# Performance work log

Hardware: AMD Instinct MI355X
Metric: run time of the kernel (lower is better)

The kernel has to match this reference:

```python
import jax, jax.numpy as jnp
import numpy as np

NUM_VIEW = 300
NUM_ANGLE = 12
NUM_DEPTH = 4
GRASP_MAX_WIDTH = 0.1
B, C, NS, NG = 2, 512, 2048, 2000


def generate_grasp_views(N=NUM_VIEW):
    phi = (np.sqrt(5.0) - 1.0) / 2.0  # fibonacci sphere
    idxs = jnp.arange(N, dtype=jnp.float32)
    Z = (2.0 * idxs + 1.0) / N - 1.0
    r = jnp.sqrt(jnp.maximum(1.0 - Z * Z, 0.0))
    X = r * jnp.cos(2.0 * jnp.pi * idxs * phi)
    Y = r * jnp.sin(2.0 * jnp.pi * idxs * phi)
    return jnp.stack([X, Y, Z], -1)  # [N,3]


def viewpoint_params_to_matrix(towards, angle):
    # towards [...,3], angle [...]
    ax = towards
    zero = jnp.zeros_like(ax[..., 0])
    ay = jnp.stack([-ax[..., 1], ax[..., 0], zero], -1)
    ynorm = jnp.linalg.norm(ay, axis=-1, keepdims=True)
    ay = jnp.where(ynorm == 0, jnp.array([0.0, 1.0, 0.0], ax.dtype), ay)
    ax = ax / jnp.linalg.norm(ax, axis=-1, keepdims=True)
    ay = ay / jnp.linalg.norm(ay, axis=-1, keepdims=True)
    az = jnp.cross(ax, ay)
    c, s = jnp.cos(angle), jnp.sin(angle)
    one = jnp.ones_like(c)
    R1 = jnp.stack([one, zero * 0 + jnp.zeros_like(c), jnp.zeros_like(c),
                    jnp.zeros_like(c), c, -s,
                    jnp.zeros_like(c), s, c], -1).reshape(angle.shape + (3, 3))
    R2 = jnp.stack([ax, ay, az], -1)  # axes as columns
    return R2 @ R1


def conv1d(x, w, b):
    # 1x1 Conv1d == channel matmul. x [B,Ci,N], w [Co,Ci]
    return jnp.einsum('oi,bin->bon', w, x) + b[None, :, None]


def knn1(q, ref):
    # K=1 nearest neighbor indices of q [Nq,3] in ref [Nr,3]
    d = (jnp.sum(q * q, -1, keepdims=True) + jnp.sum(ref * ref, -1)[None, :]
         - 2.0 * q @ ref.T)
    return jnp.argmin(d, axis=-1)


def normalize_tensor(t, eps=1e-8):
    mx = jnp.max(t, -1, keepdims=True)
    mn = jnp.min(t, -1, keepdims=True)
    return (t - mn) / (mx - mn + eps)


def _process_one(seed_xyz, pose, gpoints, gscores, gwidths, views, views_rot):
    R, t = pose[:, :3], pose[:, 3]
    gp_trans = gpoints @ R.T + t                      # [Ng,3]
    gv_trans = views @ R.T                            # [V,3]
    gv_rot_trans = jnp.einsum('ij,vjk->vik', R, views_rot)  # [V,3,3]
    view_inds = knn1(views, gv_trans)                 # [V]
    gv_rot_trans = gv_rot_trans[view_inds]            # [V,3,3]
    nn_inds = knn1(seed_xyz, gp_trans)                # [Ns]
    gp_out = gp_trans[nn_inds]                        # [Ns,3]
    # gather seed dim first (Ns<Ng) then reindex views; axes independent
    sc = gscores[nn_inds][:, view_inds]               # [Ns,V,A,D]
    wd = gwidths[nn_inds][:, view_inds]
    rot = jnp.broadcast_to(gv_rot_trans[None], (seed_xyz.shape[0],) + gv_rot_trans.shape)
    return gp_out, rot, sc, wd


def setup_inputs() -> dict:
    key = jax.random.key(0)
    ks = jax.random.split(key, 16)
    seed_features = jax.random.normal(ks[0], (B, C, NS), jnp.float32)
    point_clouds = jax.random.normal(ks[1], (B, NS, 3), jnp.float32) * 0.2
    Rq = np.linalg.qr(np.asarray(jax.random.normal(ks[2], (B, 3, 3))))[0].astype(np.float32)
    trans = jax.random.normal(ks[3], (B, 3, 1), jnp.float32) * 0.1
    object_pose = jnp.concatenate([jnp.asarray(Rq), trans], -1)  # [B,3,4]
    grasp_points = jax.random.normal(ks[4], (B, NG, 3), jnp.float32) * 0.2
    grasp_labels = jax.random.uniform(ks[5], (B, NG, NUM_VIEW, NUM_ANGLE, NUM_DEPTH)) * 1.2 - 0.2
    grasp_offsets = jax.random.uniform(ks[6], (B, NG, NUM_VIEW, NUM_ANGLE, NUM_DEPTH)) * 0.15
    w = lambda k, co, ci: jax.random.normal(k, (co, ci), jnp.float32) * 0.05
    bz = lambda co: jnp.zeros((co,), jnp.float32)
    return {
        'seed_features': seed_features, 'point_clouds': point_clouds,
        'object_pose': object_pose, 'grasp_points': grasp_points,
        'grasp_labels': grasp_labels, 'grasp_offsets': grasp_offsets,
        'aw1_w': w(ks[7], C, C), 'aw1_b': bz(C),
        'aw2_w': w(ks[8], C, C), 'aw2_b': bz(C),
        'aw3_w': w(ks[9], NUM_VIEW, C), 'aw3_b': bz(NUM_VIEW),
        'sw1_w': w(ks[10], C, C), 'sw1_b': bz(C),
        'sw2_w': w(ks[11], NUM_DEPTH * NUM_ANGLE * 2, C), 'sw2_b': bz(NUM_DEPTH * NUM_ANGLE * 2),
    }


def reference(seed_features, point_clouds, object_pose, grasp_points,
              grasp_labels, grasp_offsets, aw1_w, aw1_b, aw2_w, aw2_b,
              aw3_w, aw3_b, sw1_w, sw1_b, sw2_w, sw2_b):
    Bx, Cx, Ns = seed_features.shape
    # --- ApproachNet (eval branch) ---
    res = jax.nn.relu(conv1d(seed_features, aw1_w, aw1_b))
    res = jax.nn.relu(conv1d(res, aw2_w, aw2_b))
    view_scores = conv1d(res, aw3_w, aw3_b).transpose(0, 2, 1)  # [B,Ns,V]
    top_view_inds = jnp.argmax(view_scores, -1)                 # [B,Ns]
    views = generate_grasp_views(NUM_VIEW)
    vp_xyz = views[top_view_inds]                               # [B,Ns,3]
    vp_rot = viewpoint_params_to_matrix(-vp_xyz, jnp.zeros(vp_xyz.shape[:-1], vp_xyz.dtype))
    # --- SWADNet ---
    f = jax.nn.relu(conv1d(res, sw1_w, sw1_b))
    f = conv1d(f, sw2_w, sw2_b)
    f = f.reshape(Bx, 2, NUM_ANGLE, NUM_DEPTH, Ns).transpose(0, 1, 4, 2, 3)
    grasp_score_pred = f[:, 0]   # [B,Ns,A,D]
    grasp_width_pred = f[:, 1]
    # --- process_grasp_labels (vmapped over batch) ---
    views_rot = viewpoint_params_to_matrix(-views, jnp.zeros((NUM_VIEW,), views.dtype))
    gp, rot, sc, wd = jax.vmap(_process_one, in_axes=(0, 0, 0, 0, 0, None, None))(
        point_clouds, object_pose, grasp_points, grasp_labels, grasp_offsets, views, views_rot)
    gmask = (sc <= 0.6) & (sc > 0)
    graspness = normalize_tensor(
        gmask.astype(jnp.float32).reshape(Bx, Ns, NUM_VIEW, -1).mean(-1))  # [B,Ns,V]
    label_mask = (sc > 0) & (wd <= GRASP_MAX_WIDTH)
    sc = jnp.where(label_mask, sc, 0.0)
    # --- match_grasp_view_and_label ---
    bi = jnp.arange(Bx)[:, None]
    ni = jnp.arange(Ns)[None, :]
    top_rot = rot[bi, ni, top_view_inds]  # [B,Ns,3,3]
    top_sc = sc[bi, ni, top_view_inds]    # [B,Ns,A,D]
    top_wd = wd[bi, ni, top_view_inds]
    u_max = jnp.max(top_sc)
    po = top_sc > 0
    safe = jnp.where(po, top_sc, 1.0)
    u_min = jnp.min(jnp.where(po, top_sc, jnp.inf))
    new_sc = jnp.log(u_max / safe) / (jnp.log(u_max / u_min) + 1e-8)
    top_sc = jnp.where(po, new_sc, top_sc)
    return (view_scores, vp_rot, grasp_score_pred, grasp_width_pred,
            top_rot, top_sc, top_wd, graspness, gp)
```

## Files before the change

kernel.cpp:

```cpp
#include <hip/hip_runtime.h>
#include <math.h>

#define NV 300
#define NA 12
#define ND 4
#define NB 2
#define NC 512
#define NSD 2048
#define NGP 2000
#define ROWLEN 14400

__global__ void k_setup(float* __restrict__ views, float* __restrict__ views_rot,
                        int* __restrict__ mmx) {
  int i = threadIdx.x;
  if (i == 0) { mmx[0] = 0; mmx[1] = 0x7f800000; }
  if (i >= NV) return;
  float fi = (float)i;
  float Z = (2.0f * fi + 1.0f) / 300.0f - 1.0f;
  float r = sqrtf(fmaxf(1.0f - Z * Z, 0.0f));
  float ang = (6.28318530717958647692f * fi) * 0.61803398874989484820f;
  float X = r * cosf(ang);
  float Y = r * sinf(ang);
  views[i * 3 + 0] = X; views[i * 3 + 1] = Y; views[i * 3 + 2] = Z;
  float ax0 = -X, ax1 = -Y, ax2 = -Z;
  float ay0 = -ax1, ay1 = ax0, ay2 = 0.f;
  float ynorm = sqrtf(ay0 * ay0 + ay1 * ay1 + ay2 * ay2);
  if (ynorm == 0.f) { ay0 = 0.f; ay1 = 1.f; ay2 = 0.f; }
  float an = sqrtf(ax0 * ax0 + ax1 * ax1 + ax2 * ax2);
  ax0 /= an; ax1 /= an; ax2 /= an;
  float ayn = sqrtf(ay0 * ay0 + ay1 * ay1 + ay2 * ay2);
  ay0 /= ayn; ay1 /= ayn; ay2 /= ayn;
  float az0 = ax1 * ay2 - ax2 * ay1;
  float az1 = ax2 * ay0 - ax0 * ay2;
  float az2 = ax0 * ay1 - ax1 * ay0;
  float* m = views_rot + i * 9;
  m[0] = ax0; m[1] = ay0; m[2] = az0;
  m[3] = ax1; m[4] = ay1; m[5] = az1;
  m[6] = ax2; m[7] = ay2; m[8] = az2;
}

__global__ void __launch_bounds__(512) k_batch_setup(
    const float* __restrict__ pose, const float* __restrict__ views,
    const float* __restrict__ views_rot, int* __restrict__ view_inds,
    float* __restrict__ Rsel) {
  int b = blockIdx.x, tid = threadIdx.x;
  __shared__ float R[9];
  __shared__ float gv[NV][3];
  __shared__ float gvr[NV];
  if (tid < 9) R[tid] = pose[b * 12 + (tid / 3) * 4 + (tid % 3)];
  __syncthreads();
  if (tid < NV) {
    float vx = views[tid * 3], vy = views[tid * 3 + 1], vz = views[tid * 3 + 2];
    float x = R[0] * vx + R[1] * vy + R[2] * vz;
    float y = R[3] * vx + R[4] * vy + R[5] * vz;
    float z = R[6] * vx + R[7] * vy + R[8] * vz;
    gv[tid][0] = x; gv[tid][1] = y; gv[tid][2] = z;
    gvr[tid] = x * x + y * y + z * z;
  }
  __syncthreads();
  if (tid < NV) {
    float qx = views[tid * 3], qy = views[tid * 3 + 1], qz = views[tid * 3 + 2];
    float qq = qx * qx + qy * qy + qz * qz;
    float best = INFINITY; int bi = 0;
    for (int u = 0; u < NV; u++) {
      float dot = qx * gv[u][0] + qy * gv[u][1] + qz * gv[u][2];
      float d = qq + gvr[u] - 2.f * dot;
      if (d < best) { best = d; bi = u; }
    }
    view_inds[b * NV + tid] = bi;
    const float* vr = views_rot + bi * 9;
    float* o = Rsel + (b * NV + tid) * 9;
    for (int i = 0; i < 3; i++)
      for (int j = 0; j < 3; j++)
        o[i * 3 + j] = R[i * 3 + 0] * vr[0 + j] + R[i * 3 + 1] * vr[3 + j] + R[i * 3 + 2] * vr[6 + j];
  }
}

__global__ void k_gp_trans(const float* __restrict__ pose,
                           const float* __restrict__ gpoints,
                           float* __restrict__ gpt, float* __restrict__ grr) {
  int idx = blockIdx.x * 256 + threadIdx.x;
  if (idx >= NB * NGP) return;
  int b = idx / NGP;
  const float* P = pose + b * 12;
  float px = gpoints[(size_t)idx * 3 + 0];
  float py = gpoints[(size_t)idx * 3 + 1];
  float pz = gpoints[(size_t)idx * 3 + 2];
  float x = P[0] * px + P[1] * py + P[2] * pz + P[3];
  float y = P[4] * px + P[5] * py + P[6] * pz + P[7];
  float z = P[8] * px + P[9] * py + P[10] * pz + P[11];
  gpt[(size_t)idx * 3 + 0] = x;
  gpt[(size_t)idx * 3 + 1] = y;
  gpt[(size_t)idx * 3 + 2] = z;
  grr[idx] = x * x + y * y + z * z;
}

__global__ void __launch_bounds__(256) k_nn(
    const float* __restrict__ pc, const float* __restrict__ gpt,
    const float* __restrict__ grr, int* __restrict__ nn_inds,
    float* __restrict__ out_gp) {
  int b = blockIdx.y;
  int s = blockIdx.x * 256 + threadIdx.x;
  __shared__ float gx[NGP], gy[NGP], gz[NGP], gr[NGP];
  for (int i = threadIdx.x; i < NGP; i += 256) {
    gx[i] = gpt[((size_t)b * NGP + i) * 3 + 0];
    gy[i] = gpt[((size_t)b * NGP + i) * 3 + 1];
    gz[i] = gpt[((size_t)b * NGP + i) * 3 + 2];
    gr[i] = grr[b * NGP + i];
  }
  __syncthreads();
  float qx = pc[((size_t)b * NSD + s) * 3 + 0];
  float qy = pc[((size_t)b * NSD + s) * 3 + 1];
  float qz = pc[((size_t)b * NSD + s) * 3 + 2];
  float qq = qx * qx + qy * qy + qz * qz;
  float best = INFINITY; int bi = 0;
  for (int i = 0; i < NGP; i++) {
    float dot = qx * gx[i] + qy * gy[i] + qz * gz[i];
    float d = qq + gr[i] - 2.f * dot;
    if (d < best) { best = d; bi = i; }
  }
  nn_inds[b * NSD + s] = bi;
  out_gp[((size_t)b * NSD + s) * 3 + 0] = gx[bi];
  out_gp[((size_t)b * NSD + s) * 3 + 1] = gy[bi];
  out_gp[((size_t)b * NSD + s) * 3 + 2] = gz[bi];
}

template <bool RELU, bool GUARD_M>
__global__ void __launch_bounds__(256) gemm_k(
    const float* __restrict__ W, const float* __restrict__ X,
    const float* __restrict__ bias, float* __restrict__ Y,
    int O, int Cin, int N) {
  int b = blockIdx.z;
  const float* Xb = X + (size_t)b * Cin * N;
  float* Yb = Y + (size_t)b * O * N;
  int m0 = blockIdx.y * 64, n0 = blockIdx.x * 64;
  __shared__ float As[16][68];
  __shared__ float Bs[16][64];
  int tid = threadIdx.x;
  int mW = tid >> 2, kW = (tid & 3) * 4;
  int kX = tid >> 4, nX = (tid & 15) * 4;
  int ty = tid >> 4, tx = tid & 15;
  float acc[4][4] = {};
  for (int k0 = 0; k0 < Cin; k0 += 16) {
    float4 wv;
    if (!GUARD_M || (m0 + mW) < O)
      wv = *(const float4*)&W[(size_t)(m0 + mW) * Cin + k0 + kW];
    else
      wv = make_float4(0.f, 0.f, 0.f, 0.f);
    As[kW + 0][mW] = wv.x; As[kW + 1][mW] = wv.y;
    As[kW + 2][mW] = wv.z; As[kW + 3][mW] = wv.w;
    *(float4*)&Bs[kX][nX] = *(const float4*)&Xb[(size_t)(k0 + kX) * N + n0 + nX];
    __syncthreads();
#pragma unroll
    for (int kk = 0; kk < 16; kk++) {
      float4 a = *(const float4*)&As[kk][ty << 2];
      float4 bv = *(const float4*)&Bs[kk][tx << 2];
      acc[0][0] = fmaf(a.x, bv.x, acc[0][0]); acc[0][1] = fmaf(a.x, bv.y, acc[0][1]);
      acc[0][2] = fmaf(a.x, bv.z, acc[0][2]); acc[0][3] = fmaf(a.x, bv.w, acc[0][3]);
      acc[1][0] = fmaf(a.y, bv.x, acc[1][0]); acc[1][1] = fmaf(a.y, bv.y, acc[1][1]);
      acc[1][2] = fmaf(a.y, bv.z, acc[1][2]); acc[1][3] = fmaf(a.y, bv.w, acc[1][3]);
      acc[2][0] = fmaf(a.z, bv.x, acc[2][0]); acc[2][1] = fmaf(a.z, bv.y, acc[2][1]);
      acc[2][2] = fmaf(a.z, bv.z, acc[2][2]); acc[2][3] = fmaf(a.z, bv.w, acc[2][3]);
      acc[3][0] = fmaf(a.w, bv.x, acc[3][0]); acc[3][1] = fmaf(a.w, bv.y, acc[3][1]);
      acc[3][2] = fmaf(a.w, bv.z, acc[3][2]); acc[3][3] = fmaf(a.w, bv.w, acc[3][3]);
    }
    __syncthreads();
  }
#pragma unroll
  for (int i = 0; i < 4; i++) {
    int m = m0 + ty * 4 + i;
    if (GUARD_M && m >= O) break;
    float bi = bias[m];
    float4 v;
    v.x = acc[i][0] + bi; v.y = acc[i][1] + bi;
    v.z = acc[i][2] + bi; v.w = acc[i][3] + bi;
    if (RELU) {
      v.x = fmaxf(v.x, 0.f); v.y = fmaxf(v.y, 0.f);
      v.z = fmaxf(v.z, 0.f); v.w = fmaxf(v.w, 0.f);
    }
    *(float4*)&Yb[(size_t)m * N + n0 + (tx << 2)] = v;
  }
}

__global__ void __launch_bounds__(256) k_argmax(
    const float* __restrict__ vs_t, const float* __restrict__ views_rot,
    const float* __restrict__ Rsel, int* __restrict__ tv_inds,
    float* __restrict__ o_vprot, float* __restrict__ o_trot) {
  int b = blockIdx.y;
  int n = blockIdx.x * 256 + threadIdx.x;
  const float* src = vs_t + (size_t)b * NV * NSD + n;
  float best = src[0]; int bi = 0;
  for (int v = 1; v < NV; v++) {
    float val = src[(size_t)v * NSD];
    if (val > best) { best = val; bi = v; }
  }
  tv_inds[b * NSD + n] = bi;
  const float* vr = views_rot + bi * 9;
  float* o1 = o_vprot + ((size_t)b * NSD + n) * 9;
  const float* rs = Rsel + (b * NV + bi) * 9;
  float* o4 = o_trot + ((size_t)b * NSD + n) * 9;
#pragma unroll
  for (int i = 0; i < 9; i++) { o1[i] = vr[i]; o4[i] = rs[i]; }
}

__global__ void k_transpose_vs(const float* __restrict__ vs_t, float* __restrict__ out) {
  __shared__ float tile[32][33];
  int b = blockIdx.z;
  int v0 = blockIdx.x * 32, n0 = blockIdx.y * 32;
  const float* src = vs_t + (size_t)b * NV * NSD;
  for (int i = threadIdx.y; i < 32; i += 8) {
    int v = v0 + i;
    if (v < NV) tile[i][threadIdx.x] = src[(size_t)v * NSD + n0 + threadIdx.x];
  }
  __syncthreads();
  for (int i = threadIdx.y; i < 32; i += 8) {
    int n = n0 + i;
    int v = v0 + threadIdx.x;
    if (v < NV) out[((size_t)b * NSD + n) * NV + v] = tile[threadIdx.x][i];
  }
}

__global__ void __launch_bounds__(256) k_f2(const float* __restrict__ f2,
                                            float* __restrict__ gsp,
                                            float* __restrict__ gwp) {
  __shared__ float tile[96][65];
  int b = blockIdx.y, n0 = blockIdx.x * 64;
  const float* src = f2 + (size_t)b * 96 * NSD;
  for (int idx = threadIdx.x; idx < 96 * 64; idx += 256) {
    int ch = idx >> 6, j = idx & 63;
    tile[ch][j] = src[(size_t)ch * NSD + n0 + j];
  }
  __syncthreads();
  for (int idx = threadIdx.x; idx < 64 * 48; idx += 256) {
    int j = idx / 48, ad = idx % 48;
    size_t o = ((size_t)b * NSD + n0 + j) * 48 + ad;
    gsp[o] = tile[ad][j];
    gwp[o] = tile[48 + ad][j];
  }
}

__global__ void __launch_bounds__(256) k_grasp(
    const float* __restrict__ gscores, const float* __restrict__ goffsets,
    const int* __restrict__ nn_inds, const int* __restrict__ tv_inds,
    const int* __restrict__ view_inds, float* __restrict__ o_grsp,
    float* __restrict__ o_twd, float* __restrict__ raw) {
  int b = blockIdx.y, s = blockIdx.x, tid = threadIdx.x;
  int nn = nn_inds[b * NSD + s];
  int tv = tv_inds[b * NSD + s];
  int vit = view_inds[b * NV + tv];
  const float* srow = gscores + ((size_t)(b * NGP + nn)) * ROWLEN;
  const float* wrow = goffsets + ((size_t)(b * NGP + nn)) * ROWLEN;
  if (tid < 48) {
    float sc = srow[vit * 48 + tid];
    float wd = wrow[vit * 48 + tid];
    bool m = (sc > 0.f) && (wd <= 0.1f);
    o_twd[((size_t)b * NSD + s) * 48 + tid] = wd;
    raw[((size_t)b * NSD + s) * 48 + tid] = m ? sc : 0.f;
  }
  __shared__ float g[NV];
  for (int v = tid; v < NV; v += 256) {
    int vv = view_inds[b * NV + v];
    const float4* p = (const float4*)(srow + vv * 48);
    int cnt = 0;
#pragma unroll
    for (int q = 0; q < 12; q++) {
      float4 x = p[q];
      cnt += (x.x > 0.f && x.x <= 0.6f);
      cnt += (x.y > 0.f && x.y <= 0.6f);
      cnt += (x.z > 0.f && x.z <= 0.6f);
      cnt += (x.w > 0.f && x.w <= 0.6f);
    }
    g[v] = (float)cnt / 48.0f;
  }
  __syncthreads();
  float mx = -INFINITY, mn = INFINITY;
  for (int v = tid; v < NV; v += 256) { mx = fmaxf(mx, g[v]); mn = fminf(mn, g[v]); }
  for (int off = 32; off; off >>= 1) {
    mx = fmaxf(mx, __shfl_down(mx, off));
    mn = fminf(mn, __shfl_down(mn, off));
  }
  __shared__ float wmx[4], wmn[4];
  int wid = tid >> 6, lane = tid & 63;
  if (lane == 0) { wmx[wid] = mx; wmn[wid] = mn; }
  __syncthreads();
  if (tid == 0) {
    mx = fmaxf(fmaxf(wmx[0], wmx[1]), fmaxf(wmx[2], wmx[3]));
    mn = fminf(fminf(wmn[0], wmn[1]), fminf(wmn[2], wmn[3]));
    wmx[0] = mx; wmn[0] = mn;
  }
  __syncthreads();
  mx = wmx[0]; mn = wmn[0];
  float denom = mx - mn + 1e-8f;
  float* og = o_grsp + ((size_t)b * NSD + s) * NV;
  for (int v = tid; v < NV; v += 256) og[v] = (g[v] - mn) / denom;
}

__global__ void __launch_bounds__(256) k_reduce(const float* __restrict__ raw,
                                                int n, int* __restrict__ mmx) {
  float mx = -INFINITY, mn = INFINITY;
  for (int i = blockIdx.x * 256 + threadIdx.x; i < n; i += gridDim.x * 256) {
    float v = raw[i];
    mx = fmaxf(mx, v);
    if (v > 0.f) mn = fminf(mn, v);
  }
  for (int off = 32; off; off >>= 1) {
    mx = fmaxf(mx, __shfl_down(mx, off));
    mn = fminf(mn, __shfl_down(mn, off));
  }
  __shared__ float smx[4], smn[4];
  int wid = threadIdx.x >> 6, lane = threadIdx.x & 63;
  if (lane == 0) { smx[wid] = mx; smn[wid] = mn; }
  __syncthreads();
  if (threadIdx.x == 0) {
    mx = fmaxf(fmaxf(smx[0], smx[1]), fmaxf(smx[2], smx[3]));
    mn = fminf(fminf(smn[0], smn[1]), fminf(smn[2], smn[3]));
    atomicMax(&mmx[0], __float_as_int(mx));
    if (mn != INFINITY) atomicMin(&mmx[1], __float_as_int(mn));
  }
}

__global__ void k_topsc(const float* __restrict__ raw, const int* __restrict__ mmx,
                        float* __restrict__ out, int n) {
  int i = blockIdx.x * 256 + threadIdx.x;
  if (i >= n) return;
  float sc = raw[i];
  float umax = __int_as_float(mmx[0]);
  float umin = __int_as_float(mmx[1]);
  float denom = logf(umax / umin) + 1e-8f;
  float val = logf(umax / sc) / denom;
  out[i] = (sc > 0.f) ? val : sc;
}

extern "C" void kernel_launch(void* const* d_in, const int* in_sizes, int n_in,
                              void* d_out, int out_size, void* d_ws, size_t ws_size,
                              hipStream_t stream) {
  const float* seed_features = (const float*)d_in[0];
  const float* point_clouds  = (const float*)d_in[1];
  const float* object_pose   = (const float*)d_in[2];
  const float* grasp_points  = (const float*)d_in[3];
  const float* grasp_labels  = (const float*)d_in[4];
  const float* grasp_offsets = (const float*)d_in[5];
  const float* aw1_w = (const float*)d_in[6];
  const float* aw1_b = (const float*)d_in[7];
  const float* aw2_w = (const float*)d_in[8];
  const float* aw2_b = (const float*)d_in[9];
  const float* aw3_w = (const float*)d_in[10];
  const float* aw3_b = (const float*)d_in[11];
  const float* sw1_w = (const float*)d_in[12];
  const float* sw1_b = (const float*)d_in[13];
  const float* sw2_w = (const float*)d_in[14];
  const float* sw2_b = (const float*)d_in[15];

  float* out = (float*)d_out;
  float* o_vs    = out;
  float* o_vprot = o_vs + NB * NSD * NV;
  float* o_gsp   = o_vprot + NB * NSD * 9;
  float* o_gwp   = o_gsp + NB * NSD * 48;
  float* o_trot  = o_gwp + NB * NSD * 48;
  float* o_tsc   = o_trot + NB * NSD * 9;
  float* o_twd   = o_tsc + NB * NSD * 48;
  float* o_grsp  = o_twd + NB * NSD * 48;
  float* o_gp    = o_grsp + NB * NSD * NV;

  float* w = (float*)d_ws;
  float* res1 = w; w += NB * NC * NSD;
  float* res2 = w; w += NB * NC * NSD;
  float* vs_t = w; w += NB * NV * NSD;
  float* f2   = w; w += NB * 96 * NSD;
  float* views = w; w += 960;
  float* views_rot = w; w += 2720;
  float* gpt = w; w += NB * NGP * 3;
  float* grr = w; w += NB * NGP;
  float* Rsel = w; w += NB * NV * 9;
  float* raw  = w; w += NB * NSD * 48;
  int* view_inds = (int*)w; w += NB * NV;
  int* nn_inds   = (int*)w; w += NB * NSD;
  int* tv_inds   = (int*)w; w += NB * NSD;
  int* mmx       = (int*)w; w += 8;

  k_setup<<<1, 512, 0, stream>>>(views, views_rot, mmx);
  k_batch_setup<<<NB, 512, 0, stream>>>(object_pose, views, views_rot, view_inds, Rsel);
  k_gp_trans<<<(NB * NGP + 255) / 256, 256, 0, stream>>>(object_pose, grasp_points, gpt, grr);
  k_nn<<<dim3(NSD / 256, NB), 256, 0, stream>>>(point_clouds, gpt, grr, nn_inds, o_gp);

  gemm_k<true, false><<<dim3(NSD / 64, NC / 64, NB), 256, 0, stream>>>(
      aw1_w, seed_features, aw1_b, res1, NC, NC, NSD);
  gemm_k<true, false><<<dim3(NSD / 64, NC / 64, NB), 256, 0, stream>>>(
      aw2_w, res1, aw2_b, res2, NC, NC, NSD);
  gemm_k<false, true><<<dim3(NSD / 64, (NV + 63) / 64, NB), 256, 0, stream>>>(
      aw3_w, res2, aw3_b, vs_t, NV, NC, NSD);
  gemm_k<true, false><<<dim3(NSD / 64, NC / 64, NB), 256, 0, stream>>>(
      sw1_w, res2, sw1_b, res1, NC, NC, NSD);
  gemm_k<false, true><<<dim3(NSD / 64, (96 + 63) / 64, NB), 256, 0, stream>>>(
      sw2_w, res1, sw2_b, f2, 96, NC, NSD);

  k_argmax<<<dim3(NSD / 256, NB), 256, 0, stream>>>(vs_t, views_rot, Rsel, tv_inds,
                                                    o_vprot, o_trot);
  k_transpose_vs<<<dim3((NV + 31) / 32, NSD / 32, NB), dim3(32, 8), 0, stream>>>(vs_t, o_vs);
  k_f2<<<dim3(NSD / 64, NB), 256, 0, stream>>>(f2, o_gsp, o_gwp);
  k_grasp<<<dim3(NSD, NB), 256, 0, stream>>>(grasp_labels, grasp_offsets, nn_inds,
                                             tv_inds, view_inds, o_grsp, o_twd, raw);
  k_reduce<<<256, 256, 0, stream>>>(raw, NB * NSD * 48, mmx);
  k_topsc<<<(NB * NSD * 48 + 255) / 256, 256, 0, stream>>>(raw, mmx, o_tsc, NB * NSD * 48);
}
```

Baseline: 706.5 us.

## Use 128x64 GEMM tiles, split kNN search across threads, cache view indices

Adds a gemm128 kernel in which each thread computes an 8x4 tile with register prefetch of the next k-slice, and uses it for the four large 1x1-conv GEMMs to raise arithmetic intensity per shared-memory load. The nearest-neighbour kernel now packs each point as a float4 (xyz plus squared norm) and gives each query to 8 threads that each scan a 250-point chunk, then merges them in shared memory. This gives many more blocks and shorter serial loops. k_grasp stages view_inds in shared memory instead of re-reading global memory. The larger GEMM tiles halve the block count per GEMM, which may reduce occupancy.

```diff
diff --git a/kernel.cpp b/kernel.cpp
--- a/kernel.cpp
+++ b/kernel.cpp
@@ -78,7 +78,7 @@
 
 __global__ void k_gp_trans(const float* __restrict__ pose,
                            const float* __restrict__ gpoints,
-                           float* __restrict__ gpt, float* __restrict__ grr) {
+                           float4* __restrict__ gpt4) {
   int idx = blockIdx.x * 256 + threadIdx.x;
   if (idx >= NB * NGP) return;
   int b = idx / NGP;
@@ -89,40 +89,125 @@
   float x = P[0] * px + P[1] * py + P[2] * pz + P[3];
   float y = P[4] * px + P[5] * py + P[6] * pz + P[7];
   float z = P[8] * px + P[9] * py + P[10] * pz + P[11];
-  gpt[(size_t)idx * 3 + 0] = x;
-  gpt[(size_t)idx * 3 + 1] = y;
-  gpt[(size_t)idx * 3 + 2] = z;
-  grr[idx] = x * x + y * y + z * z;
+  gpt4[idx] = make_float4(x, y, z, x * x + y * y + z * z);
 }
 
 __global__ void __launch_bounds__(256) k_nn(
-    const float* __restrict__ pc, const float* __restrict__ gpt,
-    const float* __restrict__ grr, int* __restrict__ nn_inds,
-    float* __restrict__ out_gp) {
+    const float* __restrict__ pc, const float4* __restrict__ gpt4,
+    int* __restrict__ nn_inds, float* __restrict__ out_gp) {
   int b = blockIdx.y;
-  int s = blockIdx.x * 256 + threadIdx.x;
-  __shared__ float gx[NGP], gy[NGP], gz[NGP], gr[NGP];
-  for (int i = threadIdx.x; i < NGP; i += 256) {
-    gx[i] = gpt[((size_t)b * NGP + i) * 3 + 0];
-    gy[i] = gpt[((size_t)b * NGP + i) * 3 + 1];
-    gz[i] = gpt[((size_t)b * NGP + i) * 3 + 2];
-    gr[i] = grr[b * NGP + i];
-  }
-  __syncthreads();
+  int s0 = blockIdx.x * 32;
+  int tid = threadIdx.x;
+  __shared__ float4 pts[NGP];
+  for (int i = tid; i < NGP; i += 256) pts[i] = gpt4[b * NGP + i];
+  __syncthreads();
+  int sl = tid & 31, chunk = tid >> 5;
+  int s = s0 + sl;
   float qx = pc[((size_t)b * NSD + s) * 3 + 0];
   float qy = pc[((size_t)b * NSD + s) * 3 + 1];
   float qz = pc[((size_t)b * NSD + s) * 3 + 2];
   float qq = qx * qx + qy * qy + qz * qz;
-  float best = INFINITY; int bi = 0;
-  for (int i = 0; i < NGP; i++) {
-    float dot = qx * gx[i] + qy * gy[i] + qz * gz[i];
-    float d = qq + gr[i] - 2.f * dot;
+  int i0 = chunk * 250;
+  float best = INFINITY; int bi = i0;
+  for (int i = i0; i < i0 + 250; i++) {
+    float4 p = pts[i];
+    float d = qq + p.w - 2.f * (qx * p.x + qy * p.y + qz * p.z);
     if (d < best) { best = d; bi = i; }
   }
-  nn_inds[b * NSD + s] = bi;
-  out_gp[((size_t)b * NSD + s) * 3 + 0] = gx[bi];
-  out_gp[((size_t)b * NSD + s) * 3 + 1] = gy[bi];
-  out_gp[((size_t)b * NSD + s) * 3 + 2] = gz[bi];
+  __shared__ float rb[8][33];
+  __shared__ int ri[8][33];
+  rb[chunk][sl] = best; ri[chunk][sl] = bi;
+  __syncthreads();
+  if (tid < 32) {
+    float bb = INFINITY; int ii = 0;
+    for (int c = 0; c < 8; c++) {
+      float v = rb[c][tid];
+      if (v < bb) { bb = v; ii = ri[c][tid]; }
+    }
+    nn_inds[b * NSD + s0 + tid] = ii;
+    float4 p = pts[ii];
+    out_gp[((size_t)b * NSD + s0 + tid) * 3 + 0] = p.x;
+    out_gp[((size_t)b * NSD + s0 + tid) * 3 + 1] = p.y;
+    out_gp[((size_t)b * NSD + s0 + tid) * 3 + 2] = p.z;
+  }
+}
+
+template <bool RELU, bool GUARD_M>
+__global__ void __launch_bounds__(256) gemm128(
+    const float* __restrict__ W, const float* __restrict__ X,
+    const float* __restrict__ bias, float* __restrict__ Y,
+    int O, int Cin, int N) {
+  int b = blockIdx.z;
+  const float* Xb = X + (size_t)b * Cin * N;
+  float* Yb = Y + (size_t)b * O * N;
+  int m0 = blockIdx.y * 128, n0 = blockIdx.x * 64;
+  __shared__ float As[16][132];
+  __shared__ float Bs[16][64];
+  int tid = threadIdx.x;
+  int mW = tid >> 1;
+  int kW = (tid & 1) * 8;
+  int kX = tid >> 4, nX = (tid & 15) * 4;
+  int ty = tid >> 4, tx = tid & 15;
+  bool okm = !GUARD_M || (m0 + mW) < O;
+  float4 a0, a1, bv;
+  {
+    const float* wp = &W[(size_t)(m0 + mW) * Cin + kW];
+    a0 = okm ? *(const float4*)wp : make_float4(0.f, 0.f, 0.f, 0.f);
+    a1 = okm ? *(const float4*)(wp + 4) : make_float4(0.f, 0.f, 0.f, 0.f);
+    bv = *(const float4*)&Xb[(size_t)kX * N + n0 + nX];
+  }
+  float acc[8][4] = {};
+  for (int k0 = 0; k0 < Cin; k0 += 16) {
+    __syncthreads();
+    As[kW + 0][mW] = a0.x; As[kW + 1][mW] = a0.y;
+    As[kW + 2][mW] = a0.z; As[kW + 3][mW] = a0.w;
+    As[kW + 4][mW] = a1.x; As[kW + 5][mW] = a1.y;
+    As[kW + 6][mW] = a1.z; As[kW + 7][mW] = a1.w;
+    *(float4*)&Bs[kX][nX] = bv;
+    __syncthreads();
+    if (k0 + 16 < Cin) {
+      const float* wp = &W[(size_t)(m0 + mW) * Cin + k0 + 16 + kW];
+      a0 = okm ? *(const float4*)wp : make_float4(0.f, 0.f, 0.f, 0.f);
+      a1 = okm ? *(const float4*)(wp + 4) : make_float4(0.f, 0.f, 0.f, 0.f);
+      bv = *(const float4*)&Xb[(size_t)(k0 + 16 + kX) * N + n0 + nX];
+    }
+#pragma unroll
+    for (int kk = 0; kk < 16; kk++) {
+      float4 x0 = *(const float4*)&As[kk][ty * 8];
+      float4 x1 = *(const float4*)&As[kk][ty * 8 + 4];
+      float4 y = *(const float4*)&Bs[kk][tx * 4];
+      acc[0][0] = fmaf(x0.x, y.x, acc[0][0]); acc[0][1] = fmaf(x0.x, y.y, acc[0][1]);
+      acc[0][2] = fmaf(x0.x, y.z, acc[0][2]); acc[0][3] = fmaf(x0.x, y.w, acc[0][3]);
+      acc[1][0] = fmaf(x0.y, y.x, acc[1][0]); acc[1][1] = fmaf(x0.y, y.y, acc[1][1]);
+      acc[1][2] = fmaf(x0.y, y.z, acc[1][2]); acc[1][3] = fmaf(x0.y, y.w, acc[1][3]);
+      acc[2][0] = fmaf(x0.z, y.x, acc[2][0]); acc[2][1] = fmaf(x0.z, y.y, acc[2][1]);
+      acc[2][2] = fmaf(x0.z, y.z, acc[2][2]); acc[2][3] = fmaf(x0.z, y.w, acc[2][3]);
+      acc[3][0] = fmaf(x0.w, y.x, acc[3][0]); acc[3][1] = fmaf(x0.w, y.y, acc[3][1]);
+      acc[3][2] = fmaf(x0.w, y.z, acc[3][2]); acc[3][3] = fmaf(x0.w, y.w, acc[3][3]);
+      acc[4][0] = fmaf(x1.x, y.x, acc[4][0]); acc[4][1] = fmaf(x1.x, y.y, acc[4][1]);
+      acc[4][2] = fmaf(x1.x, y.z, acc[4][2]); acc[4][3] = fmaf(x1.x, y.w, acc[4][3]);
+      acc[5][0] = fmaf(x1.y, y.x, acc[5][0]); acc[5][1] = fmaf(x1.y, y.y, acc[5][1]);
+      acc[5][2] = fmaf(x1.y, y.z, acc[5][2]); acc[5][3] = fmaf(x1.y, y.w, acc[5][3]);
+      acc[6][0] = fmaf(x1.z, y.x, acc[6][0]); acc[6][1] = fmaf(x1.z, y.y, acc[6][1]);
+      acc[6][2] = fmaf(x1.z, y.z, acc[6][2]); acc[6][3] = fmaf(x1.z, y.w, acc[6][3]);
+      acc[7][0] = fmaf(x1.w, y.x, acc[7][0]); acc[7][1] = fmaf(x1.w, y.y, acc[7][1]);
+      acc[7][2] = fmaf(x1.w, y.z, acc[7][2]); acc[7][3] = fmaf(x1.w, y.w, acc[7][3]);
+    }
+  }
+#pragma unroll
+  for (int i = 0; i < 8; i++) {
+    int m = m0 + ty * 8 + i;
+    if (GUARD_M && m >= O) break;
+    float bi = bias[m];
+    float4 v;
+    v.x = acc[i][0] + bi; v.y = acc[i][1] + bi;
+    v.z = acc[i][2] + bi; v.w = acc[i][3] + bi;
+    if (RELU) {
+      v.x = fmaxf(v.x, 0.f); v.y = fmaxf(v.y, 0.f);
+      v.z = fmaxf(v.z, 0.f); v.w = fmaxf(v.w, 0.f);
+    }
+    *(float4*)&Yb[(size_t)m * N + n0 + (tx << 2)] = v;
+  }
 }
 
 template <bool RELU, bool GUARD_M>
@@ -245,9 +330,12 @@
     const int* __restrict__ view_inds, float* __restrict__ o_grsp,
     float* __restrict__ o_twd, float* __restrict__ raw) {
   int b = blockIdx.y, s = blockIdx.x, tid = threadIdx.x;
+  __shared__ int vi[NV];
+  for (int v = tid; v < NV; v += 256) vi[v] = view_inds[b * NV + v];
+  __syncthreads();
   int nn = nn_inds[b * NSD + s];
   int tv = tv_inds[b * NSD + s];
-  int vit = view_inds[b * NV + tv];
+  int vit = vi[tv];
   const float* srow = gscores + ((size_t)(b * NGP + nn)) * ROWLEN;
   const float* wrow = goffsets + ((size_t)(b * NGP + nn)) * ROWLEN;
   if (tid < 48) {
@@ -259,7 +347,7 @@
   }
   __shared__ float g[NV];
   for (int v = tid; v < NV; v += 256) {
-    int vv = view_inds[b * NV + v];
+    int vv = vi[v];
     const float4* p = (const float4*)(srow + vv * 48);
     int cnt = 0;
 #pragma unroll
@@ -369,8 +457,7 @@
   float* f2   = w; w += NB * 96 * NSD;
   float* views = w; w += 960;
   float* views_rot = w; w += 2720;
-  float* gpt = w; w += NB * NGP * 3;
-  float* grr = w; w += NB * NGP;
+  float4* gpt4 = (float4*)w; w += NB * NGP * 4;
   float* Rsel = w; w += NB * NV * 9;
   float* raw  = w; w += NB * NSD * 48;
   int* view_inds = (int*)w; w += NB * NV;
@@ -380,18 +467,18 @@
 
   k_setup<<<1, 512, 0, stream>>>(views, views_rot, mmx);
   k_batch_setup<<<NB, 512, 0, stream>>>(object_pose, views, views_rot, view_inds, Rsel);
-  k_gp_trans<<<(NB * NGP + 255) / 256, 256, 0, stream>>>(object_pose, grasp_points, gpt, grr);
-  k_nn<<<dim3(NSD / 256, NB), 256, 0, stream>>>(point_clouds, gpt, grr, nn_inds, o_gp);
-
-  gemm_k<true, false><<<dim3(NSD / 64, NC / 64, NB), 256, 0, stream>>>(
+  k_gp_trans<<<(NB * NGP + 255) / 256, 256, 0, stream>>>(object_pose, grasp_points, gpt4);
+  k_nn<<<dim3(NSD / 32, NB), 256, 0, stream>>>(point_clouds, gpt4, nn_inds, o_gp);
+
+  gemm128<true, false><<<dim3(NSD / 64, NC / 128, NB), 256, 0, stream>>>(
       aw1_w, seed_features, aw1_b, res1, NC, NC, NSD);
-  gemm_k<true, false><<<dim3(NSD / 64, NC / 64, NB), 256, 0, stream>>>(
+  gemm128<true, false><<<dim3(NSD / 64, NC / 128, NB), 256, 0, stream>>>(
       aw2_w, res1, aw2_b, res2, NC, NC, NSD);
-  gemm_k<false, true><<<dim3(NSD / 64, (NV + 63) / 64, NB), 256, 0, stream>>>(
+  gemm128<false, true><<<dim3(NSD / 64, (NV + 127) / 128, NB), 256, 0, stream>>>(
       aw3_w, res2, aw3_b, vs_t, NV, NC, NSD);
-  gemm_k<true, false><<<dim3(NSD / 64, NC / 64, NB), 256, 0, stream>>>(
+  gemm128<true, false><<<dim3(NSD / 64, NC / 128, NB), 256, 0, stream>>>(
       sw1_w, res2, sw1_b, res1, NC, NC, NSD);
-  gemm_k<false, true><<<dim3(NSD / 64, (96 + 63) / 64, NB), 256, 0, stream>>>(
+  gemm_k<false, true><<<dim3(NSD / 64, 2, NB), 256, 0, stream>>>(
       sw2_w, res1, sw2_b, f2, 96, NC, NSD);
 
   k_argmax<<<dim3(NSD / 256, NB), 256, 0, stream>>>(vs_t, views_rot, Rsel, tv_inds,
```

New measurement: 655.5 us. -7.2%, faster.
